# Kernel optimization log

Measured on AMD Instinct MI355X. Metric: run time of the kernel, lower is better.

Reference implementation:

```python
import jax, jax.numpy as jnp
import numpy as np

B, S, D, H = 2, 2048, 1024, 16
HEAD_DIM = D // H
THETA = 10000.0


def setup_inputs() -> dict:
    key = jax.random.key(0)
    kx, kq, kk, kv, ko = jax.random.split(key, 5)
    w_scale = jnp.float32(D ** -0.5)  # keep logits O(1)
    return {
        "x": jax.random.normal(kx, (B, S, D), dtype=jnp.float32),
        "WQ": jax.random.normal(kq, (D, D), dtype=jnp.float32) * w_scale,
        "WK": jax.random.normal(kk, (D, D), dtype=jnp.float32) * w_scale,
        "WV": jax.random.normal(kv, (D, D), dtype=jnp.float32) * w_scale,
        "WO": jax.random.normal(ko, (D, D), dtype=jnp.float32) * w_scale,
        "token_positions": jnp.arange(S, dtype=jnp.int32),
    }


def _rope(x, pos, theta):
    # x: [B, H, S, dh]; pos: [S]. Interleaved (even, odd) pair rotation.
    dh = x.shape[-1]
    inv_freq = theta ** (-jnp.arange(0, dh, 2, dtype=jnp.float32) / dh)  # [dh/2]
    ang = pos.astype(jnp.float32)[:, None] * inv_freq                    # [S, dh/2]
    cos, sin = jnp.cos(ang), jnp.sin(ang)
    x1, x2 = x[..., 0::2], x[..., 1::2]
    r1 = x1 * cos - x2 * sin
    r2 = x1 * sin + x2 * cos
    return jnp.stack([r1, r2], axis=-1).reshape(x.shape)


def reference(x, WQ, WK, WV, WO, token_positions):
    Bs, Ss, Dm = x.shape
    dh = Dm // H
    # QKV projections (Linear with no bias, y = x @ W.T), split heads -> [B,H,S,dh]
    q = (x @ WQ.T).reshape(Bs, Ss, H, dh).transpose(0, 2, 1, 3)
    k = (x @ WK.T).reshape(Bs, Ss, H, dh).transpose(0, 2, 1, 3)
    v = (x @ WV.T).reshape(Bs, Ss, H, dh).transpose(0, 2, 1, 3)
    q = _rope(q, token_positions, THETA)
    k = _rope(k, token_positions, THETA)
    scores = jnp.einsum("bhqd,bhkd->bhqk", q, k) * jnp.float32(dh ** -0.5)
    causal = jnp.tril(jnp.ones((Ss, Ss), dtype=bool))
    scores = jnp.where(causal, scores, jnp.finfo(scores.dtype).min)
    attn = jax.nn.softmax(scores, axis=-1)
    out = jnp.einsum("bhqk,bhkd->bhqd", attn, v)
    out = out.transpose(0, 2, 1, 3).reshape(Bs, Ss, Dm)
    return out @ WO.T
```

## Files before the change

### kernel.cpp

```cpp
#include <hip/hip_runtime.h>
#include <hip/hip_bf16.h>


#define S_LEN 2048
#define NEG_SENT -30000.0f

typedef __attribute__((ext_vector_type(8))) short short8;
typedef __attribute__((ext_vector_type(4))) float f32x4;
typedef unsigned int u32;
typedef unsigned short u16;

static __device__ __forceinline__ float bf2f(u16 u) {
  union { u32 i; float f; } v; v.i = ((u32)u) << 16; return v.f;
}
static __device__ __forceinline__ u16 f2bf(float f) {
  union { float f; u32 i; } v; v.f = f;
  u32 u = v.i;
  u32 r = (u + 0x7fffu + ((u >> 16) & 1u)) >> 16;
  return (u16)r;
}
static __device__ __forceinline__ u32 cvtpk(float a, float b) {
  u32 r;
  asm("v_cvt_pk_bf16_f32 %0, %1, %2" : "=v"(r) : "v"(a), "v"(b));
  return r;
}

static __device__ __forceinline__ void glds16(const void* g, void* l) {
  __builtin_amdgcn_global_load_lds((const __attribute__((address_space(1))) u32*)g,
                                   (__attribute__((address_space(3))) u32*)l, 16, 0, 0);
}

__global__ void convert_kernel(const float* __restrict__ x, const float* __restrict__ wq,
                               const float* __restrict__ wk, const float* __restrict__ wv,
                               const float* __restrict__ wo, u16* __restrict__ xb,
                               u16* __restrict__ wb) {
  int i = blockIdx.x * blockDim.x + threadIdx.x;
  const float* src; u16* dst; int off;
  if (i < 1048576) { src = x; dst = xb; off = i; }
  else {
    int j = i - 1048576;
    int widx = j >> 18;
    off = j & 262143;
    src = (widx == 0) ? wq : (widx == 1) ? wk : (widx == 2) ? wv : wo;
    dst = wb + (size_t)widx * 1048576;
  }
  float4 v = ((const float4*)src)[off];
  ushort4 o;
  o.x = f2bf(v.x); o.y = f2bf(v.y); o.z = f2bf(v.z); o.w = f2bf(v.w);
  ((ushort4*)dst)[off] = o;
}

__global__ void rope_kernel(u32* __restrict__ Qb, u32* __restrict__ Kb,
                            const int* __restrict__ pos) {
  int i = blockIdx.x * blockDim.x + threadIdx.x;
  int c = i & 511;
  int rowi = i >> 9;
  int s = rowi & (S_LEN - 1);
  int ip = c & 31;
  float p = (float)pos[s];
  float ang = p * __builtin_exp2f((float)ip * -0.41524101186f);
  float sn, cs;
  sincosf(ang, &sn, &cs);
  u32 v = Qb[i];
  float x1 = bf2f((u16)(v & 0xffff)), x2 = bf2f((u16)(v >> 16));
  float r1 = x1 * cs - x2 * sn, r2 = x1 * sn + x2 * cs;
  Qb[i] = (u32)f2bf(r1) | ((u32)f2bf(r2) << 16);
  v = Kb[i];
  x1 = bf2f((u16)(v & 0xffff)); x2 = bf2f((u16)(v >> 16));
  r1 = x1 * cs - x2 * sn; r2 = x1 * sn + x2 * cs;
  Kb[i] = (u32)f2bf(r1) | ((u32)f2bf(r2) << 16);
}

template <int OUTMODE>
__global__ __launch_bounds__(256, 2) void gemm_bt(const u16* __restrict__ A,
                                                  const u16* __restrict__ B,
                                                  u16* __restrict__ o0, u16* __restrict__ o1,
                                                  u16* __restrict__ o2, float* __restrict__ oF,
                                                  int K) {
  __shared__ __align__(16) u16 AsBs[2 * 128 * 64];
  u16* const As = AsBs;
  u16* const Bs = AsBs + 128 * 64;
  const int tid = threadIdx.x, w = tid >> 6, l = tid & 63, l15 = l & 15, l4 = l >> 4;
  const int wr = w >> 1, wc = w & 1;
  const int m0 = blockIdx.y << 7, n0 = blockIdx.x << 7;
  const int r = tid >> 3;
  const int swcol = ((tid & 7) << 4) ^ ((r & 7) << 4);
  const char* Ag = (const char*)A + (((size_t)(m0 + r) * K) << 1) + swcol;
  const char* Bg = (const char*)B + (((size_t)(n0 + r) * K) << 1) + swcol;
  char* AsW = (char*)As + (w << 10);
  char* BsW = (char*)Bs + (w << 10);
  const size_t rowskip = ((size_t)32 * K) << 1;
  f32x4 acc[4][4] = {};
  for (int k0 = 0; k0 < K; k0 += 64) {
    __syncthreads();
    const size_t kb = (size_t)k0 << 1;
#pragma unroll
    for (int i = 0; i < 4; i++) {
      glds16(Ag + kb + (size_t)i * rowskip, AsW + i * 4096);
      glds16(Bg + kb + (size_t)i * rowskip, BsW + i * 4096);
    }
    __syncthreads();
#pragma unroll
    for (int kk = 0; kk < 2; kk++) {
      short8 a[4], b[4];
#pragma unroll
      for (int m = 0; m < 4; m++) {
        int row = (wr << 6) + (m << 4) + l15;
        a[m] = *(const short8*)((const char*)As + row * 128 +
                                (((kk << 6) + (l4 << 4)) ^ ((row & 7) << 4)));
      }
#pragma unroll
      for (int n = 0; n < 4; n++) {
        int row = (wc << 6) + (n << 4) + l15;
        b[n] = *(const short8*)((const char*)Bs + row * 128 +
                                (((kk << 6) + (l4 << 4)) ^ ((row & 7) << 4)));
      }
#pragma unroll
      for (int m = 0; m < 4; m++)
#pragma unroll
        for (int n = 0; n < 4; n++)
          acc[m][n] = __builtin_amdgcn_mfma_f32_16x16x32_bf16(a[m], b[n], acc[m][n], 0, 0, 0);
    }
  }
  if (OUTMODE == 0 && n0 >= 2048) {
    __syncthreads();
    u16* T = AsBs;
#pragma unroll
    for (int m = 0; m < 4; m++)
#pragma unroll
      for (int n = 0; n < 4; n++) {
        int ct = (wc << 6) + (n << 4) + l15;
#pragma unroll
        for (int j = 0; j < 4; j++) {
          int rt = (wr << 6) + (m << 4) + (l4 << 2) + j;
          T[rt * 128 + (ct ^ (((rt >> 6) & 1) << 1))] = f2bf(acc[m][n][j]);
        }
      }
    __syncthreads();
    const int d = tid >> 1, sh = tid & 1;
    const int dr = d ^ (sh << 1);
    const int bb = m0 >> 11;
    const int colv = (n0 & 1023) + d;
    const int row = (((bb << 4) | (colv >> 6)) << 6) | (colv & 63);
    u16* dst = o2 + ((size_t)row << 11) + (m0 & (S_LEN - 1)) + (sh << 6);
#pragma unroll
    for (int k8 = 0; k8 < 8; k8++) {
      u16 tmp[8];
#pragma unroll
      for (int e = 0; e < 8; e++) tmp[e] = T[((sh << 6) + (k8 << 3) + e) * 128 + dr];
      *(uint4*)(dst + (k8 << 3)) = *(const uint4*)tmp;
    }
    return;
  }
#pragma unroll
  for (int m = 0; m < 4; m++) {
    int grow_b = m0 + (wr << 6) + (m << 4) + (l4 << 2);
#pragma unroll
    for (int n = 0; n < 4; n++) {
      int gcol = n0 + (wc << 6) + (n << 4) + l15;
#pragma unroll
      for (int j = 0; j < 4; j++) {
        int grow = grow_b + j;
        float v = acc[m][n][j];
        if (OUTMODE == 0) {
          u16* base = (gcol < 1024) ? o0 : o1;
          base[((size_t)grow << 10) + (gcol & 1023)] = f2bf(v);
        } else {
          oF[((size_t)grow << 10) + gcol] = v;
        }
      }
    }
  }
}

__global__ __launch_bounds__(512, 1) void attn_kernel(const u16* __restrict__ Q,
                                                      const u16* __restrict__ K,
                                                      const u16* __restrict__ Vt,
                                                      u16* __restrict__ O) {
  extern __shared__ __align__(16) char smem[];
  const int tid = threadIdx.x, w = tid >> 6, l = tid & 63, l15 = l & 15, g = l >> 4;
  const int grp = w >> 2, w4 = w & 3;
  const int i = blockIdx.x;
  const int xcd = i & 7, slot = i >> 3;
  const int bh = ((slot >> 3) << 3) | xcd;
  const int p = slot & 7;
  const int b = bh >> 4, h = bh & 15;
  const float C2 = 0.125f * 1.44269504089f;
  const float MC = 20.f * C2;
  const int swz = (l15 & 7) << 4;

  const int gt = tid & 255;
  const int r = gt >> 3;
  const int swc = ((gt & 7) << 4) ^ ((r & 7) << 4);
  const char* Kg = (const char*)K + ((size_t)(b * S_LEN + r) << 11) + (h << 7) + swc;
  const char* Vg = (const char*)Vt + ((size_t)((bh << 6) + r) << 12) + swc;
  char* const KsG = smem + (grp << 15);
  char* const VsG = smem + (grp << 15) + 16384;
  char* const Pw = smem + 65536 + (w << 11);
  float* const oMrg = (float*)smem;
  float* const lMrg = (float*)(smem + 65536);

#define STAGE(T, BSEL)                                              \
  do {                                                              \
    char* kd = KsG + ((BSEL) << 13) + (w4 << 10);                   \
    char* vd = VsG + ((BSEL) << 13) + (w4 << 10);                   \
    const char* ks = Kg + ((size_t)(T) << 17);                      \
    const char* vs = Vg + ((T) << 7);                               \
    glds16(ks, kd);                                                 \
    glds16(ks + (32 << 11), kd + 4096);                             \
    glds16(vs, vd);                                                 \
    glds16(vs + ((size_t)32 << 12), vd + 4096);                     \
  } while (0)

  auto run_qt = [&](int qt) {
    const int q0 = qt << 7;
    const int nr = qt + 1;

    short8 aQ[2][2];
    {
      const int qrow0 = q0 + (w4 << 5) + l15;
      const u16* qp = Q + (((size_t)(b * S_LEN + qrow0)) << 10) + (h << 6) + (g << 3);
      aQ[0][0] = *(const short8*)qp;
      aQ[0][1] = *(const short8*)(qp + 32);
      aQ[1][0] = *(const short8*)(qp + (16 << 10));
      aQ[1][1] = *(const short8*)(qp + (16 << 10) + 32);
    }
    f32x4 o[2][4] = {};
    float l_r[2] = {0.f, 0.f};

    STAGE(grp, 0);
    __syncthreads();

    for (int rr = 0; rr < nr; ++rr) {
      const int bsel = rr & 1;
      if (rr + 1 < nr) STAGE(2 * (rr + 1) + grp, bsel ^ 1);
      const char* Kbuf = KsG + (bsel << 13);
      const char* Vbuf = VsG + (bsel << 13);
      const int t = 2 * rr + grp;
      const bool domask = (rr == nr - 1);

      f32x4 s[2][4] = {};
#pragma unroll
      for (int kk = 0; kk < 2; ++kk) {
        short8 aK[4];
#pragma unroll
        for (int n = 0; n < 4; ++n) {
          int row = (n << 4) + l15;
          aK[n] = *(const short8*)(Kbuf + row * 128 + (((kk << 6) + (g << 4)) ^ swz));
        }
        __builtin_amdgcn_s_setprio(1);
#pragma unroll
        for (int n = 0; n < 4; ++n) {
          s[0][n] = __builtin_amdgcn_mfma_f32_16x16x32_bf16(aK[n], aQ[0][kk], s[0][n], 0, 0, 0);
          s[1][n] = __builtin_amdgcn_mfma_f32_16x16x32_bf16(aK[n], aQ[1][kk], s[1][n], 0, 0, 0);
        }
        __builtin_amdgcn_s_setprio(0);
      }
      if (domask) {
#pragma unroll
        for (int qs = 0; qs < 2; ++qs) {
          int qg = q0 + (w4 << 5) + (qs << 4) + l15;
#pragma unroll
          for (int n = 0; n < 4; ++n)
#pragma unroll
            for (int jj = 0; jj < 4; ++jj) {
              int key = (t << 6) + (n << 4) + (g << 2) + jj;
              if (key > qg) s[qs][n][jj] = NEG_SENT;
            }
        }
      }
      short8 aP[2][2];
#pragma unroll
      for (int qs = 0; qs < 2; ++qs) {
        float rs = 0.f;
        u32 pk[8];
#pragma unroll
        for (int n = 0; n < 4; ++n) {
          float p0 = __builtin_exp2f(s[qs][n][0] * C2 - MC);
          float p1 = __builtin_exp2f(s[qs][n][1] * C2 - MC);
          float p2 = __builtin_exp2f(s[qs][n][2] * C2 - MC);
          float p3 = __builtin_exp2f(s[qs][n][3] * C2 - MC);
          rs += (p0 + p1) + (p2 + p3);
          pk[2 * n] = cvtpk(p0, p1);
          pk[2 * n + 1] = cvtpk(p2, p3);
        }
        l_r[qs] += rs;
        char* pr = Pw + l15 * 128;
#pragma unroll
        for (int n = 0; n < 4; ++n) {
          uint2 pv;
          pv.x = pk[2 * n];
          pv.y = pk[2 * n + 1];
          *(uint2*)(pr + (((n << 5) + (g << 3)) ^ swz)) = pv;
        }
#pragma unroll
        for (int kk = 0; kk < 2; ++kk)
          aP[qs][kk] = *(const short8*)(Pw + l15 * 128 + ((((kk << 6) + (g << 4))) ^ swz));
      }
#pragma unroll
      for (int kk = 0; kk < 2; ++kk) {
        int co = (kk << 6) + (g << 4);
        __builtin_amdgcn_s_setprio(1);
#pragma unroll
        for (int nd = 0; nd < 4; ++nd) {
          int row = (nd << 4) + l15;
          short8 bV = *(const short8*)(Vbuf + row * 128 + (co ^ swz));
          o[0][nd] = __builtin_amdgcn_mfma_f32_16x16x32_bf16(aP[0][kk], bV, o[0][nd], 0, 0, 0);
          o[1][nd] = __builtin_amdgcn_mfma_f32_16x16x32_bf16(aP[1][kk], bV, o[1][nd], 0, 0, 0);
        }
        __builtin_amdgcn_s_setprio(0);
      }
      __syncthreads();
    }

    if (grp == 1) {
      float* ob = oMrg + (w4 << 11);
#pragma unroll
      for (int qs = 0; qs < 2; ++qs)
#pragma unroll
        for (int nd = 0; nd < 4; ++nd)
          *(f32x4*)(ob + (((qs << 2) | nd) << 8) + (l << 2)) = o[qs][nd];
      float* lb = lMrg + (w4 << 7);
      lb[l] = l_r[0];
      lb[64 + l] = l_r[1];
    }
    __syncthreads();
    if (grp == 0) {
      float* ob = oMrg + (w4 << 11);
      float* lb = lMrg + (w4 << 7);
#pragma unroll
      for (int qs = 0; qs < 2; ++qs) {
        float lsum = l_r[qs] + lb[(qs << 6) + l];
        lsum += __shfl_xor(lsum, 16);
        lsum += __shfl_xor(lsum, 32);
        float linv = 1.f / lsum;
        f32x4 oB[4];
#pragma unroll
        for (int nd = 0; nd < 4; ++nd)
          oB[nd] = *(const f32x4*)(ob + (((qs << 2) | nd) << 8) + (l << 2));
#pragma unroll
        for (int jj = 0; jj < 4; ++jj) {
          float lo = __shfl(linv, (g << 2) + jj, 16);
          int qg = q0 + (w4 << 5) + (qs << 4) + (g << 2) + jj;
          u16* orow = O + (((size_t)(b * S_LEN + qg)) << 10) + (h << 6) + l15;
#pragma unroll
          for (int nd = 0; nd < 4; ++nd)
            orow[nd << 4] = f2bf((o[qs][nd][jj] + oB[nd][jj]) * lo);
        }
      }
    }
    __syncthreads();
  };

  run_qt(p);
  run_qt(15 - p);
#undef STAGE
}

extern "C" void kernel_launch(void* const* d_in, const int* in_sizes, int n_in,
                              void* d_out, int out_size, void* d_ws, size_t ws_size,
                              hipStream_t stream) {
  (void)in_sizes; (void)n_in; (void)out_size; (void)ws_size;
  const float* x = (const float*)d_in[0];
  const float* wq = (const float*)d_in[1];
  const float* wk = (const float*)d_in[2];
  const float* wv = (const float*)d_in[3];
  const float* wo = (const float*)d_in[4];
  const int* pos = (const int*)d_in[5];
  char* ws = (char*)d_ws;
  u16* xb = (u16*)ws;
  u16* wb = (u16*)(ws + ((size_t)8 << 20));
  u16* Qb = (u16*)(ws + ((size_t)16 << 20));
  u16* Kb = (u16*)(ws + ((size_t)24 << 20));
  u16* Vtg = (u16*)(ws + ((size_t)32 << 20));
  u16* Ab = (u16*)(ws + ((size_t)40 << 20));
  float* out = (float*)d_out;

  convert_kernel<<<8192, 256, 0, stream>>>(x, wq, wk, wv, wo, xb, wb);
  dim3 g1(24, 32);
  gemm_bt<0><<<g1, 256, 0, stream>>>(xb, wb, Qb, Kb, Vtg, nullptr, 1024);
  rope_kernel<<<8192, 256, 0, stream>>>((u32*)Qb, (u32*)Kb, pos);
  attn_kernel<<<256, 512, 81920, stream>>>(Qb, Kb, Vtg, Ab);
  dim3 g3(8, 32);
  gemm_bt<1><<<g3, 256, 0, stream>>>(Ab, wb + (size_t)3 * 1048576, nullptr, nullptr, nullptr,
                                     out, 1024);
}
```

Before: 108.6 us.

## Triple-buffer K/V tiles in attention with partial vmcnt waits

Moves the attention kernel's K/V shared-memory staging from double to triple buffering. Each iteration prefetches the tile two steps ahead and waits only for older loads (vmcnt(4)) before the barrier, instead of draining all memory traffic. This is meant to hide global-to-LDS latency better. In exchange, LDS use per block grows from 80KB to 112KB, which can limit occupancy, and the hand-written waitcnt and barrier sequence must match the load count exactly.

```diff
diff --git a/kernel.cpp b/kernel.cpp
--- a/kernel.cpp
+++ b/kernel.cpp
@@ -194,16 +194,16 @@
   const int swc = ((gt & 7) << 4) ^ ((r & 7) << 4);
   const char* Kg = (const char*)K + ((size_t)(b * S_LEN + r) << 11) + (h << 7) + swc;
   const char* Vg = (const char*)Vt + ((size_t)((bh << 6) + r) << 12) + swc;
-  char* const KsG = smem + (grp << 15);
-  char* const VsG = smem + (grp << 15) + 16384;
-  char* const Pw = smem + 65536 + (w << 11);
+  char* const KsG = smem + grp * 49152;
+  char* const VsG = smem + grp * 49152 + 24576;
+  char* const Pw = smem + 98304 + (w << 11);
   float* const oMrg = (float*)smem;
-  float* const lMrg = (float*)(smem + 65536);
+  float* const lMrg = (float*)(smem + 98304);
 
 #define STAGE(T, BSEL)                                              \
   do {                                                              \
-    char* kd = KsG + ((BSEL) << 13) + (w4 << 10);                   \
-    char* vd = VsG + ((BSEL) << 13) + (w4 << 10);                   \
+    char* kd = KsG + (BSEL) * 8192 + (w4 << 10);                    \
+    char* vd = VsG + (BSEL) * 8192 + (w4 << 10);                    \
     const char* ks = Kg + ((size_t)(T) << 17);                      \
     const char* vs = Vg + ((T) << 7);                               \
     glds16(ks, kd);                                                 \
@@ -229,13 +229,25 @@
     float l_r[2] = {0.f, 0.f};
 
     STAGE(grp, 0);
-    __syncthreads();
-
+    if (nr > 1) {
+      STAGE(2 + grp, 1);
+      __builtin_amdgcn_sched_barrier(0);
+      asm volatile("s_waitcnt vmcnt(4)");
+      __builtin_amdgcn_s_barrier();
+      __builtin_amdgcn_sched_barrier(0);
+    } else {
+      __syncthreads();
+    }
+
+    int cur = 0;
     for (int rr = 0; rr < nr; ++rr) {
-      const int bsel = rr & 1;
-      if (rr + 1 < nr) STAGE(2 * (rr + 1) + grp, bsel ^ 1);
-      const char* Kbuf = KsG + (bsel << 13);
-      const char* Vbuf = VsG + (bsel << 13);
+      const bool stg = (rr + 2 < nr);
+      if (stg) {
+        int b2 = (cur >= 1) ? cur - 1 : cur + 2;
+        STAGE(2 * (rr + 2) + grp, b2);
+      }
+      const char* Kbuf = KsG + cur * 8192;
+      const char* Vbuf = VsG + cur * 8192;
       const int t = 2 * rr + grp;
       const bool domask = (rr == nr - 1);
 
@@ -310,7 +322,16 @@
         }
         __builtin_amdgcn_s_setprio(0);
       }
-      __syncthreads();
+      if (rr + 1 < nr) {
+        __builtin_amdgcn_sched_barrier(0);
+        if (stg) asm volatile("s_waitcnt vmcnt(4)");
+        else     asm volatile("s_waitcnt vmcnt(0)");
+        __builtin_amdgcn_s_barrier();
+        __builtin_amdgcn_sched_barrier(0);
+      } else {
+        __syncthreads();
+      }
+      cur = (cur == 2) ? 0 : cur + 1;
     }
 
     if (grp == 1) {
@@ -380,7 +401,7 @@
   dim3 g1(24, 32);
   gemm_bt<0><<<g1, 256, 0, stream>>>(xb, wb, Qb, Kb, Vtg, nullptr, 1024);
   rope_kernel<<<8192, 256, 0, stream>>>((u32*)Qb, (u32*)Kb, pos);
-  attn_kernel<<<256, 512, 81920, stream>>>(Qb, Kb, Vtg, Ab);
+  attn_kernel<<<256, 512, 114688, stream>>>(Qb, Kb, Vtg, Ab);
   dim3 g3(8, 32);
   gemm_bt<1><<<g3, 256, 0, stream>>>(Ab, wb + (size_t)3 * 1048576, nullptr, nullptr, nullptr,
                                      out, 1024);
```

New measurement: 109.1 us. About the same (+0.5%).
